# Kernel optimization log

Measured on AMD Instinct MI355X. Metric: run time of the kernel, lower is better.

The kernel has to match this reference:

```python
import jax, jax.numpy as jnp
import numpy as np

CONF_THRES = 0.1
IOU_THRES = 0.6
MAX_DET = 300
MAX_WH = 4096.0  # class offset for non-agnostic NMS
NEG_SLOPE = 0.01  # nn.LeakyReLU default


def xywh2xyxy(p):
    xy, wh = p[..., :2], p[..., 2:4]
    return jnp.concatenate([xy - wh / 2, xy + wh / 2], axis=-1)


def pairwise_iou(a, b):
    area_a = (a[:, 2] - a[:, 0]) * (a[:, 3] - a[:, 1])
    area_b = (b[:, 2] - b[:, 0]) * (b[:, 3] - b[:, 1])
    lt = jnp.maximum(a[:, None, :2], b[None, :, :2])
    rb = jnp.minimum(a[:, None, 2:], b[None, :, 2:])
    wh = jnp.clip(rb - lt, 0.0)
    inter = wh[..., 0] * wh[..., 1]
    return inter / (area_a[:, None] + area_b[None, :] - inter + 1e-7)


def nms_single(pred):  # pred: [N, 5+nc]
    boxes = xywh2xyxy(pred[:, :4])
    scores = pred[:, 5:] * pred[:, 4:5]  # obj * cls
    conf = jnp.max(scores, axis=1)
    cls = jnp.argmax(scores, axis=1)
    conf = jnp.where(conf > CONF_THRES, conf, 0.0)
    topv, topi = jax.lax.top_k(conf, MAX_DET)
    b = boxes[topi]                      # [K,4]
    c = cls[topi]
    valid = topv > CONF_THRES
    bo = b + (c.astype(b.dtype) * MAX_WH)[:, None]  # class-offset boxes
    iou = pairwise_iou(bo, bo)           # [K,K]
    idx = jnp.arange(MAX_DET)
    def body(i, keep):
        sup = keep[i] & (iou[i] > IOU_THRES) & (idx > i)
        return keep & ~sup
    keep = jax.lax.fori_loop(0, MAX_DET, body, valid)
    return b, keep


def bilinear_sample(feat, y, x):  # feat [C,H,W], y/x [K,P] -> [C,K,P]
    C, H, W = feat.shape
    y = jnp.clip(y, 0.0, H - 1.0)
    x = jnp.clip(x, 0.0, W - 1.0)
    y0 = jnp.floor(y).astype(jnp.int32)
    x0 = jnp.floor(x).astype(jnp.int32)
    y1 = jnp.minimum(y0 + 1, H - 1)
    x1 = jnp.minimum(x0 + 1, W - 1)
    ly = y - y0
    lx = x - x0
    return (feat[:, y0, x0] * ((1 - ly) * (1 - lx))
            + feat[:, y0, x1] * ((1 - ly) * lx)
            + feat[:, y1, x0] * (ly * (1 - lx))
            + feat[:, y1, x1] * (ly * lx))


def roi_align_1x1(feat, boxes, scale):  # feat [C,H,W], boxes [K,4] xyxy (input-px)
    b = boxes * scale
    w = jnp.maximum(b[:, 2] - b[:, 0], 1.0)
    h = jnp.maximum(b[:, 3] - b[:, 1], 1.0)
    off = jnp.array([0.5, 1.5], dtype=boxes.dtype)
    xs = b[:, 0:1] + off[None, :] * (w[:, None] / 2.0)  # [K,2]
    ys = b[:, 1:2] + off[None, :] * (h[:, None] / 2.0)
    yy = ys[:, jnp.array([0, 0, 1, 1])]  # [K,4] 2x2 grid
    xx = xs[:, jnp.array([0, 1, 0, 1])]
    v = bilinear_sample(feat, yy, xx)    # [C,K,4]
    return jnp.mean(v, axis=2).T         # [K,C]


def rescale_boxes(bbox, hw, hw0):  # scale_coords + normalize by orig shape
    gain = jnp.minimum(hw[0] / hw0[0], hw[1] / hw0[1])
    pad_x = (hw[1] - hw0[1] * gain) / 2.0
    pad_y = (hw[0] - hw0[0] * gain) / 2.0
    x1 = jnp.clip((bbox[:, 0] - pad_x) / gain, 0.0, hw0[1])
    y1 = jnp.clip((bbox[:, 1] - pad_y) / gain, 0.0, hw0[0])
    x2 = jnp.clip((bbox[:, 2] - pad_x) / gain, 0.0, hw0[1])
    y2 = jnp.clip((bbox[:, 3] - pad_y) / gain, 0.0, hw0[0])
    # divide by shapes[i][0] indexed [w,h,w,h]
    return jnp.stack([x1 / hw0[1], y1 / hw0[0], x2 / hw0[1], y2 / hw0[0]], axis=1)


def setup_inputs() -> dict:
    key = jax.random.key(0)
    ks = jax.random.split(key, 10)
    B, N, NC = 8, 25500, 80
    xy = jax.random.uniform(ks[0], (B, N, 2), minval=0.0, maxval=640.0)
    wh = jax.random.uniform(ks[1], (B, N, 2), minval=8.0, maxval=160.0)
    obj = jax.random.uniform(ks[2], (B, N, 1))
    cls = jax.random.uniform(ks[3], (B, N, NC))
    preds = jnp.concatenate([xy, wh, obj, cls], axis=-1)
    feat1 = jax.random.normal(ks[4], (B, 128, 80, 80), dtype=jnp.float32)
    feat2 = jax.random.normal(ks[5], (B, 256, 40, 40), dtype=jnp.float32)
    feat3 = jax.random.normal(ks[6], (B, 512, 20, 20), dtype=jnp.float32)
    feat4 = jax.random.normal(ks[7], (B, 1024, 10, 10), dtype=jnp.float32)
    orig_hw = jnp.tile(jnp.array([[720.0, 1280.0]], dtype=jnp.float32), (B, 1))
    W1 = jax.random.normal(ks[8], (1920, 256), dtype=jnp.float32) * 0.02
    b1 = jnp.zeros((256,), dtype=jnp.float32)
    W2 = jax.random.normal(ks[9], (256, 256), dtype=jnp.float32) * 0.02
    b2 = jnp.zeros((256,), dtype=jnp.float32)
    return {"preds": preds, "feat1": feat1, "feat2": feat2, "feat3": feat3,
            "feat4": feat4, "orig_hw": orig_hw, "W1": W1, "b1": b1,
            "W2": W2, "b2": b2}


def reference(preds, feat1, feat2, feat3, feat4, orig_hw, W1, b1, W2, b2):
    preds = jax.lax.stop_gradient(preds)  # out.detach() in the original
    hw = jnp.array(feat1.shape[-2:], dtype=preds.dtype) * 8.0  # network input h,w
    boxes, keep = jax.vmap(nms_single)(preds)  # [B,K,4], [B,K]
    f1 = jax.vmap(lambda f, b: roi_align_1x1(f, b, 1.0 / 8))(feat1, boxes)
    f2 = jax.vmap(lambda f, b: roi_align_1x1(f, b, 1.0 / 16))(feat2, boxes)
    f3 = jax.vmap(lambda f, b: roi_align_1x1(f, b, 1.0 / 32))(feat3, boxes)
    f4 = jax.vmap(lambda f, b: roi_align_1x1(f, b, 1.0 / 64))(feat4, boxes)
    f = jnp.concatenate([f1, f2, f3, f4], axis=-1)  # [B,K,1920]
    h = jax.nn.leaky_relu(f @ W1 + b1, NEG_SLOPE)
    h = jax.nn.leaky_relu(h @ W2 + b2, NEG_SLOPE)   # [B,K,256]
    bb = jax.vmap(lambda b, s: rescale_boxes(b, hw, s))(boxes, orig_hw)
    out = jnp.concatenate([bb, h], axis=-1)  # [B,K,260]
    return out * keep[..., None].astype(out.dtype)
```

## Files before the change

### kernel.cpp

```cpp
#include <hip/hip_runtime.h>
#include <hip/hip_bf16.h>
#include <cstdint>
#include <cstddef>

#define NBATCH 8
#define NANCH 25500
#define MAXDET 300
#define NBINS 2048
#define NMS_BLKS 8
#define SCAT_BLKS 64
#define TRANS_BASE (NMS_BLKS + SCAT_BLKS)
#define TRANS_BLKS 376

typedef __bf16 bf16x8 __attribute__((ext_vector_type(8)));
typedef float floatx4 __attribute__((ext_vector_type(4)));
typedef unsigned long long ull;

__device__ __forceinline__ int conf_bin(float v) {
  unsigned bits = __float_as_uint(v);
  int bin = (int)((bits - 0x3D800000u) >> 14);
  return bin > (NBINS - 1) ? (NBINS - 1) : bin;
}

#define CONF_TILE 64
__global__ __launch_bounds__(256) void conf_kernel(const float* __restrict__ preds,
                                                   float* __restrict__ conf,
                                                   int* __restrict__ cls,
                                                   int* __restrict__ ghist, int total) {
  __shared__ float s[CONF_TILE * 85];
  int base = blockIdx.x * CONF_TILE;
  int nA = total - base; if (nA > CONF_TILE) nA = CONF_TILE;
  int n4 = (nA * 85) >> 2;
  const float4* g4 = (const float4*)(preds + (size_t)base * 85);
  float4* s4 = (float4*)s;
  for (int i = threadIdx.x; i < n4; i += 256) s4[i] = g4[i];
  __syncthreads();
  int lane16 = threadIdx.x & 15;
  int sub = threadIdx.x >> 4;
  #pragma unroll
  for (int r = 0; r < 4; ++r) {
    int a = r * 16 + sub;
    if (a < nA) {
      const float* row = s + a * 85;
      float obj = row[4];
      float best = -1.0f; int bc = 0;
      #pragma unroll
      for (int j = 0; j < 5; ++j) {
        int c = lane16 * 5 + j;
        float v = row[5 + c] * obj;
        if (v > best) { best = v; bc = c; }
      }
      #pragma unroll
      for (int m = 1; m < 16; m <<= 1) {
        float ov = __shfl_xor(best, m, 64);
        int   oc = __shfl_xor(bc,   m, 64);
        if (ov > best || (ov == best && oc < bc)) { best = ov; bc = oc; }
      }
      if (lane16 == 0) {
        int idx = base + a;
        bool pass = best > 0.1f;
        conf[idx] = pass ? best : 0.0f;
        cls[idx] = bc;
        if (pass) {
          int b = idx / NANCH;
          atomicAdd(&ghist[b * NBINS + conf_bin(best)], 1);
        }
      }
    }
  }
}

struct TransArgs {
  const float* src[6];
  __hip_bfloat16* dst[6];
  int C[6], HW[6], tx[6], tpb[6], start[6];
};

__global__ __launch_bounds__(1024) void mid_kernel(TransArgs a,
                                                   const float* __restrict__ conf,
                                                   const float* __restrict__ preds,
                                                   const int* __restrict__ clsg,
                                                   const int* __restrict__ ghist,
                                                   int* __restrict__ gcnt,
                                                   int* __restrict__ ctr2,
                                                   ull* __restrict__ gA,
                                                   ull* __restrict__ gB,
                                                   ull* __restrict__ gC,
                                                   float* __restrict__ boxesWs, int* __restrict__ keepWs,
                                                   const float* __restrict__ orig_hw,
                                                   float* __restrict__ out,
                                                   int n_trans_tiles) {
  #pragma clang fp contract(off)
  __shared__ __align__(16) char smem[69632];
  int bid = blockIdx.x;
  int t = threadIdx.y * 32 + threadIdx.x;

  if (bid >= TRANS_BASE) {
    int wv = t >> 6, l = t & 63;
    int wid = (bid - TRANS_BASE) * 16 + wv;
    int wtot = ((int)gridDim.x - TRANS_BASE) * 16;
    float* tile = (float*)(smem + wv * 4352);
    for (int gt = wid; gt < n_trans_tiles; gt += wtot) {
      int s = 0;
      #pragma unroll
      for (int i = 1; i < 6; ++i) if (gt >= a.start[i]) s = i;
      int local = gt - a.start[s];
      int C = a.C[s], HW = a.HW[s], tx0 = a.tx[s], tpb = a.tpb[s];
      int bb = local / tpb;
      int rem = local - bb * tpb;
      int p0 = (rem % tx0) * 32;
      int c0 = (rem / tx0) * 32;
      const float* inb = a.src[s] + (size_t)bb * C * HW;
      __hip_bfloat16* outb = a.dst[s] + (size_t)bb * C * HW;
      if (p0 + 32 <= HW) {
        #pragma unroll
        for (int k = 0; k < 4; ++k) {
          int cr = k * 8 + (l >> 3);
          int pr = (l & 7) * 4;
          float4 v = *(const float4*)(inb + (size_t)(c0 + cr) * HW + p0 + pr);
          float* d = tile + cr * 33 + pr;
          d[0] = v.x; d[1] = v.y; d[2] = v.z; d[3] = v.w;
        }
        asm volatile("s_waitcnt lgkmcnt(0)" ::: "memory");
        __builtin_amdgcn_sched_barrier(0);
        #pragma unroll
        for (int k = 0; k < 16; ++k) {
          int pr = k * 2 + (l >> 5);
          int cr = l & 31;
          outb[(size_t)(p0 + pr) * C + c0 + cr] = __float2bfloat16(tile[cr * 33 + pr]);
        }
      } else {
        int nvp = HW - p0;
        #pragma unroll
        for (int k = 0; k < 4; ++k) {
          int cr = k * 8 + (l >> 3);
          int pr = (l & 7) * 4;
          const float* src = inb + (size_t)(c0 + cr) * HW + p0;
          float* d = tile + cr * 33 + pr;
          #pragma unroll
          for (int j = 0; j < 4; ++j) d[j] = (pr + j < nvp) ? src[pr + j] : 0.0f;
        }
        asm volatile("s_waitcnt lgkmcnt(0)" ::: "memory");
        __builtin_amdgcn_sched_barrier(0);
        #pragma unroll
        for (int k = 0; k < 16; ++k) {
          int pr = k * 2 + (l >> 5);
          int cr = l & 31;
          if (pr < nvp) outb[(size_t)(p0 + pr) * C + c0 + cr] = __float2bfloat16(tile[cr * 33 + pr]);
        }
      }
    }
    return;
  }

  if (bid >= NMS_BLKS) {
    int hb = bid - NMS_BLKS;
    int b = hb >> 3, seg = hb & 7;
    int* s_suf = (int*)smem;
    int* shv   = (int*)(smem + 8192);
    int r[8], suf[8], rs[8];
    int w = t >> 6, lane = t & 63;
    if (t == 0) shv[0] = NBINS;
    if (t < 256) {
      #pragma unroll
      for (int k = 0; k < 8; ++k)
        r[k] = ghist[b * NBINS + (w * 8 + k) * 64 + lane];
      int bsum = 0;
      #pragma unroll
      for (int k = 0; k < 8; ++k) {
        int s = r[k];
        #pragma unroll
        for (int d = 1; d < 64; d <<= 1) {
          int o = __shfl_down(s, d, 64);
          if (lane + d < 64) s += o;
        }
        suf[k] = s - r[k];
        rs[k] = __shfl(s, 0, 64);
        bsum += rs[k];
      }
      if (lane == 0) shv[4 + w] = bsum;
    }
    __syncthreads();
    if (t < 256) {
      int p1 = shv[5], p2 = shv[6], p3 = shv[7];
      int total = shv[4] + p1 + p2 + p3;
      int target = total < 300 ? total : 300;
      int RS = (w == 0) ? (p1 + p2 + p3) : (w == 1) ? (p2 + p3) : (w == 2) ? p3 : 0;
      int run = RS;
      #pragma unroll
      for (int k = 7; k >= 0; --k) {
        int Sx = run + suf[k] + r[k];
        int Sx1 = Sx - r[k];
        int bin = (w * 8 + k) * 64 + lane;
        s_suf[bin] = Sx1;
        if (total > 0 && Sx >= target && Sx1 < target) shv[0] = bin;
        run += rs[k];
      }
    }
    __syncthreads();
    int T = shv[0];
    const int N4 = NANCH >> 2;
    int i0 = (N4 * seg) >> 3, i1 = (N4 * (seg + 1)) >> 3;
    const float4* cf4 = (const float4*)(conf + (size_t)b * NANCH);
    for (int i = i0 + t; i < i1; i += 1024) {
      float4 v4 = cf4[i];
      int ib = i * 4;
      float vv[4] = {v4.x, v4.y, v4.z, v4.w};
      #pragma unroll
      for (int q = 0; q < 4; ++q) {
        float v = vv[q];
        if (v > 0.1f) {
          int bin = conf_bin(v);
          if (bin >= T) {
            int slot = s_suf[bin] + atomicAdd(&gcnt[b * NBINS + bin], 1);
            int idx = ib + q;
            const float* p = preds + ((size_t)b * NANCH + idx) * 85;
            float cx = p[0], cy = p[1], wq = p[2], hq = p[3];
            float hw2 = wq * 0.5f, hh2 = hq * 0.5f;
            float x1 = cx - hw2, y1 = cy - hh2, x2 = cx + hw2, y2 = cy + hh2;
            int c = clsg[(size_t)b * NANCH + idx];
            size_t g = (size_t)b * NANCH + slot;
            atomicExch(&gA[g], ((ull)__float_as_uint(v) << 32) | (unsigned)(idx | (c << 20)));
            atomicExch(&gB[g], ((ull)__float_as_uint(x1) << 32) | __float_as_uint(y1));
            atomicExch(&gC[g], ((ull)__float_as_uint(x2) << 32) | __float_as_uint(y2));
          }
        }
      }
    }
    __syncthreads();
    if (t == 0) { __threadfence(); atomicAdd(&ctr2[b], 1); }
    return;
  }

  int b = bid;
  int*    s_h  = (int*)smem;
  float4* bo4  = (float4*)(smem + 8192);
  float (*bxx)[4] = (float(*)[4])(smem + 12992);
  ull   (*mask)[5] = (ull(*)[5])(smem + 17792);
  ull* keepw = (ull*)(smem + 29792);
  ull* nzrow = (ull*)(smem + 29832);
  int* shv   = (int*)(smem + 29872);

  if (t < 300) {
    bo4[t] = make_float4(0.0f, 0.0f, 0.0f, 0.0f);
    bxx[t][0] = 0.0f; bxx[t][1] = 0.0f; bxx[t][2] = 0.0f; bxx[t][3] = 0.0f;
  }
  if (t < 5) nzrow[t] = 0ULL;
  if (t == 0) { shv[0] = NBINS; shv[2] = 0; }
  {
    int r[8], suf[8], rs[8];
    int w = t >> 6, lane = t & 63;
    if (t < 256) {
      #pragma unroll
      for (int k = 0; k < 8; ++k)
        r[k] = ghist[b * NBINS + (w * 8 + k) * 64 + lane];
      int bsum = 0;
      #pragma unroll
      for (int k = 0; k < 8; ++k) {
        int s = r[k];
        #pragma unroll
        for (int d = 1; d < 64; d <<= 1) {
          int o = __shfl_down(s, d, 64);
          if (lane + d < 64) s += o;
        }
        suf[k] = s - r[k];
        rs[k] = __shfl(s, 0, 64);
        bsum += rs[k];
      }
      if (lane == 0) shv[4 + w] = bsum;
    }
    __syncthreads();
    if (t < 256) {
      int p1 = shv[5], p2 = shv[6], p3 = shv[7];
      int total = shv[4] + p1 + p2 + p3;
      int target = total < 300 ? total : 300;
      int RS = (w == 0) ? (p1 + p2 + p3) : (w == 1) ? (p2 + p3) : (w == 2) ? p3 : 0;
      int run = RS;
      #pragma unroll
      for (int k = 7; k >= 0; --k) {
        int Sx = run + suf[k] + r[k];
        int Sx1 = Sx - r[k];
        int bin = (w * 8 + k) * 64 + lane;
        s_h[bin] = Sx;
        if (total > 0 && Sx >= target && Sx1 < target) { shv[0] = bin; shv[2] = Sx; }
        run += rs[k];
      }
      if (t == 0) shv[1] = total;
    }
  }
  __syncthreads();
  int total = shv[1];
  int Kslots = shv[2];
  int nvalid = total < 300 ? total : 300;

  if (t >= nvalid && t < 300) {
    size_t bi = ((size_t)(b * 300 + t)) * 4;
    boxesWs[bi + 0] = 0.0f; boxesWs[bi + 1] = 0.0f;
    boxesWs[bi + 2] = 0.0f; boxesWs[bi + 3] = 0.0f;
  }
  if (t < 5) {
    int n = nvalid - t * 64;
    keepw[t] = (n <= 0) ? 0ULL : (n >= 64 ? ~0ULL : ((1ULL << n) - 1ULL));
  }
  if (t == 0) {
    while (atomicAdd(&ctr2[b], 0) < 8) __builtin_amdgcn_s_sleep(8);
    __threadfence();
  }
  __syncthreads();

  for (int sIdx = t; sIdx < Kslots; sIdx += 1024) {
    ull aA = atomicAdd(&gA[(size_t)b * NANCH + sIdx], 0ULL);
    float v = __uint_as_float((unsigned)(aA >> 32));
    unsigned code = (unsigned)aA;
    int id = (int)(code & 0xFFFFFu);
    int bin = conf_bin(v);
    int lo = (bin + 1 < NBINS) ? s_h[bin + 1] : 0;
    int hi = s_h[bin];
    int rank = lo;
    #pragma unroll 4
    for (int j = lo; j < hi; ++j) {
      ull aj = atomicAdd(&gA[(size_t)b * NANCH + j], 0ULL);
      float vj = __uint_as_float((unsigned)(aj >> 32));
      int ij = (int)((unsigned)aj & 0xFFFFFu);
      int gt = vj > v;
      int eq = (vj == v) & (ij < id);
      rank += gt | eq;
    }
    if (rank < 300) {
      ull pb = atomicAdd(&gB[(size_t)b * NANCH + sIdx], 0ULL);
      ull pc = atomicAdd(&gC[(size_t)b * NANCH + sIdx], 0ULL);
      float x1 = __uint_as_float((unsigned)(pb >> 32));
      float y1 = __uint_as_float((unsigned)pb);
      float x2 = __uint_as_float((unsigned)(pc >> 32));
      float y2 = __uint_as_float((unsigned)pc);
      bxx[rank][0] = x1; bxx[rank][1] = y1; bxx[rank][2] = x2; bxx[rank][3] = y2;
      size_t bi = ((size_t)(b * 300 + rank)) * 4;
      boxesWs[bi + 0] = x1; boxesWs[bi + 1] = y1;
      boxesWs[bi + 2] = x2; boxesWs[bi + 3] = y2;
      int c = (int)((code >> 20) & 0x7Fu);
      float off = (float)c * 4096.0f;
      float4 ob; ob.x = x1 + off; ob.y = y1 + off; ob.z = x2 + off; ob.w = y2 + off;
      bo4[rank] = ob;
    }
  }
  __syncthreads();

  {
    int wv2 = t >> 6, ln = t & 63;
    if (wv2 < 10) {
      int w2 = wv2 >> 1, half = wv2 & 1;
      int j = w2 * 64 + ln;
      int jc = j < 300 ? j : 0;
      float4 jb = bo4[jc];
      float ja = (jb.z - jb.x) * (jb.w - jb.y);
      bool jv = j < 300;
      int iend = w2 * 64 + 64; if (iend > 300) iend = 300;
      int i0 = half * 150, i1 = i0 + 150; if (i1 > iend) i1 = iend;
      #pragma unroll 4
      for (int i = i0; i < i1; ++i) {
        float4 ib = bo4[i];
        float ai = (ib.z - ib.x) * (ib.w - ib.y);
        float ltx = fmaxf(ib.x, jb.x);
        float lty = fmaxf(ib.y, jb.y);
        float rbx = fminf(ib.z, jb.z);
        float rby = fminf(ib.w, jb.w);
        float wx = fmaxf(rbx - ltx, 0.0f);
        float wy = fmaxf(rby - lty, 0.0f);
        float inter = wx * wy;
        float iou = inter / (ai + ja - inter + 1e-7f);
        ull bal = __ballot(jv && (j > i) && (iou > 0.6f));
        if (ln == 0) {
          mask[i][w2] = bal;
          if (bal) atomicOr(&nzrow[i >> 6], 1ULL << (i & 63));
        }
      }
    }
  }
  __syncthreads();
  if (t == 0) {
    ull kw[5], nz[5];
    #pragma unroll
    for (int w2 = 0; w2 < 5; ++w2) { kw[w2] = keepw[w2]; nz[w2] = nzrow[w2]; }
    #pragma unroll
    for (int w2 = 0; w2 < 5; ++w2) {
      ull p = kw[w2] & nz[w2];
      while (p) {
        int l2 = __builtin_ctzll(p);
        p &= p - 1;
        int i = w2 * 64 + l2;
        for (int w3 = w2; w3 < 5; ++w3) {
          ull m = mask[i][w3];
          kw[w3] &= ~m;
          if (w3 == w2) p &= ~m;
        }
      }
    }
    #pragma unroll
    for (int w2 = 0; w2 < 5; ++w2) keepw[w2] = kw[w2];
  }
  __syncthreads();
  if (t < 300) {
    int kp = (int)((keepw[t >> 6] >> (t & 63)) & 1ULL);
    keepWs[b * 300 + t] = kp;
    float oh = orig_hw[b * 2 + 0], ow = orig_hw[b * 2 + 1];
    float gain = fminf(640.0f / oh, 640.0f / ow);
    float padx = (640.0f - ow * gain) * 0.5f;
    float pady = (640.0f - oh * gain) * 0.5f;
    float x1 = fminf(fmaxf((bxx[t][0] - padx) / gain, 0.0f), ow) / ow;
    float y1 = fminf(fmaxf((bxx[t][1] - pady) / gain, 0.0f), oh) / oh;
    float x2 = fminf(fmaxf((bxx[t][2] - padx) / gain, 0.0f), ow) / ow;
    float y2 = fminf(fmaxf((bxx[t][3] - pady) / gain, 0.0f), oh) / oh;
    size_t o = ((size_t)(b * 300 + t)) * 260;
    out[o + 0] = kp ? x1 : 0.0f;
    out[o + 1] = kp ? y1 : 0.0f;
    out[o + 2] = kp ? x2 : 0.0f;
    out[o + 3] = kp ? y2 : 0.0f;
  }
}

__global__ __launch_bounds__(256) void roi_kernel(const float* __restrict__ boxes,
                                                  const __hip_bfloat16* __restrict__ fT1, const __hip_bfloat16* __restrict__ fT2,
                                                  const __hip_bfloat16* __restrict__ fT3, const __hip_bfloat16* __restrict__ fT4,
                                                  __hip_bfloat16* __restrict__ f) {
  int b = blockIdx.x & 7;
  int r = blockIdx.x >> 3;
  __shared__ int t_off[4][16];
  __shared__ float t_w[4][16];
  int t = threadIdx.x;
  const int Hs[4] = {80, 40, 20, 10};
  const int Cs[4] = {128, 256, 512, 1024};
  const float ss[4] = {0.125f, 0.0625f, 0.03125f, 0.015625f};
  size_t bbase = ((size_t)(b * 300 + r)) * 4;
  float bx0 = boxes[bbase + 0];
  float by0 = boxes[bbase + 1];
  float bx1 = boxes[bbase + 2];
  float by1 = boxes[bbase + 3];
  if (t < 64) {
    int lv = t >> 4, k = t & 15, pp = k >> 2, nb = k & 3;
    float s = ss[lv];
    int H = Hs[lv], W = Hs[lv], C = Cs[lv];
    float b0 = bx0 * s, b1 = by0 * s, b2 = bx1 * s, b3 = by1 * s;
    float w = fmaxf(b2 - b0, 1.0f), h = fmaxf(b3 - b1, 1.0f);
    const float offv[2] = {0.5f, 1.5f};
    float px = b0 + offv[pp & 1] * (w * 0.5f);
    float py = b1 + offv[pp >> 1] * (h * 0.5f);
    float y = fminf(fmaxf(py, 0.0f), (float)(H - 1));
    float x = fminf(fmaxf(px, 0.0f), (float)(W - 1));
    int y0 = (int)floorf(y), x0 = (int)floorf(x);
    int y1 = min(y0 + 1, H - 1), x1 = min(x0 + 1, W - 1);
    float ly = y - (float)y0, lx = x - (float)x0;
    int yy = (nb & 2) ? y1 : y0;
    int xx = (nb & 1) ? x1 : x0;
    float wy = (nb & 2) ? ly : (1.0f - ly);
    float wx = (nb & 1) ? lx : (1.0f - lx);
    t_off[lv][k] = (yy * W + xx) * C;
    t_w[lv][k] = wy * wx;
  }
  __syncthreads();
  const __hip_bfloat16* bases[4] = {
    fT1 + (size_t)b * 6400 * 128,
    fT2 + (size_t)b * 1600 * 256,
    fT3 + (size_t)b * 400 * 512,
    fT4 + (size_t)b * 100 * 1024
  };
  __hip_bfloat16* frow = f + (size_t)(b * 300 + r) * 1920;
  int cbase = 0;
  #pragma unroll
  for (int lv = 0; lv < 4; ++lv) {
    int C = Cs[lv];
    const __hip_bfloat16* base = bases[lv];
    for (int c = t; c < C; c += 256) {
      float acc = 0.0f;
      #pragma unroll
      for (int k = 0; k < 16; ++k)
        acc += t_w[lv][k] * __bfloat162float(base[t_off[lv][k] + c]);
      frow[cbase + c] = __float2bfloat16(acc * 0.25f);
    }
    cbase += C;
  }
}

#define GLDS16(gp, lp) __builtin_amdgcn_global_load_lds( \
    (const __attribute__((address_space(1))) unsigned int*)(gp), \
    (__attribute__((address_space(3))) unsigned int*)(lp), 16, 0, 0)

__global__ __launch_bounds__(256) void gemm_tile_kernel(const __hip_bfloat16* __restrict__ A,
                                                        const __hip_bfloat16* __restrict__ BT,
                                                        const float* __restrict__ bias,
                                                        __hip_bfloat16* __restrict__ Cb,
                                                        float* __restrict__ Cf,
                                                        const int* __restrict__ keep,
                                                        int M, int N, int K, int ldc, int coff) {
  __shared__ __hip_bfloat16 sA[2][64 * 64];
  __shared__ __hip_bfloat16 sB[2][64 * 64];
  int tid = threadIdx.x;
  int bm = blockIdx.x * 64, bn = blockIdx.y * 64;
  int wave = tid >> 6, lane = tid & 63;
  int wr = wave >> 1, wc = wave & 1;
  int idx16 = lane & 15, kb = lane >> 4;
  floatx4 acc[2][2] = {};
  int nt = K >> 6;

  auto stage = [&](int buf, int t) {
    int k0 = t << 6;
    #pragma unroll
    for (int i = 0; i < 2; ++i) {
      int c = tid + i * 256;
      int row = c >> 3, cc = c & 7;
      int scc = cc ^ (row & 7);
      GLDS16(A + (size_t)(bm + row) * K + k0 + scc * 8,
             (char*)&sA[buf][0] + c * 16);
    }
    #pragma unroll
    for (int i = 0; i < 2; ++i) {
      int c = tid + i * 256;
      int row = c >> 3, cc = c & 7;
      int scc = cc ^ (row & 7);
      GLDS16(BT + (size_t)(bn + row) * K + k0 + scc * 8,
             (char*)&sB[buf][0] + c * 16);
    }
  };

  stage(0, 0);
  asm volatile("s_waitcnt vmcnt(0)" ::: "memory");
  __syncthreads();
  int cur = 0;
  for (int t = 0; t < nt; ++t) {
    if (t + 1 < nt) stage(cur ^ 1, t + 1);
    const char* Ab = (const char*)&sA[cur][0];
    const char* Bb = (const char*)&sB[cur][0];
    #pragma unroll
    for (int s = 0; s < 2; ++s) {
      bf16x8 af[2], bg[2];
      #pragma unroll
      for (int m = 0; m < 2; ++m) {
        int row = wr * 32 + m * 16 + idx16;
        int chunk = s * 4 + kb;
        af[m] = *(const bf16x8*)(Ab + row * 128 + ((chunk ^ (row & 7)) * 16));
      }
      #pragma unroll
      for (int n = 0; n < 2; ++n) {
        int row = wc * 32 + n * 16 + idx16;
        int chunk = s * 4 + kb;
        bg[n] = *(const bf16x8*)(Bb + row * 128 + ((chunk ^ (row & 7)) * 16));
      }
      #pragma unroll
      for (int m = 0; m < 2; ++m)
        #pragma unroll
        for (int n = 0; n < 2; ++n)
          acc[m][n] = __builtin_amdgcn_mfma_f32_16x16x32_bf16(af[m], bg[n], acc[m][n], 0, 0, 0);
    }
    asm volatile("s_waitcnt vmcnt(0)" ::: "memory");
    __syncthreads();
    cur ^= 1;
  }
  int col = lane & 15, rb4 = (lane >> 4) * 4;
  #pragma unroll
  for (int m = 0; m < 2; ++m) {
    #pragma unroll
    for (int n = 0; n < 2; ++n) {
      #pragma unroll
      for (int r = 0; r < 4; ++r) {
        int orow = bm + wr * 32 + m * 16 + rb4 + r;
        int ocol = bn + wc * 32 + n * 16 + col;
        if (orow >= M) continue;
        float v = acc[m][n][r] + bias[ocol];
        v = (v >= 0.0f) ? v : 0.01f * v;
        if (Cb) Cb[(size_t)orow * N + ocol] = __float2bfloat16(v);
        if (Cf) {
          float km = keep ? (keep[orow] ? 1.0f : 0.0f) : 1.0f;
          Cf[(size_t)orow * ldc + coff + ocol] = v * km;
        }
      }
    }
  }
}

extern "C" void kernel_launch(void* const* d_in, const int* in_sizes, int n_in,
                              void* d_out, int out_size, void* d_ws, size_t ws_size,
                              hipStream_t stream) {
  (void)in_sizes; (void)n_in; (void)out_size; (void)ws_size;
  const float* preds  = (const float*)d_in[0];
  const float* feat1  = (const float*)d_in[1];
  const float* feat2  = (const float*)d_in[2];
  const float* feat3  = (const float*)d_in[3];
  const float* feat4  = (const float*)d_in[4];
  const float* orighw = (const float*)d_in[5];
  const float* W1     = (const float*)d_in[6];
  const float* b1     = (const float*)d_in[7];
  const float* W2     = (const float*)d_in[8];
  const float* b2     = (const float*)d_in[9];
  float* out = (float*)d_out;

  char* ws = (char*)d_ws;
  size_t off = 0;
  auto alloc = [&](size_t bytes) -> void* {
    void* p = ws + off;
    off = (off + bytes + 255) & ~(size_t)255;
    return p;
  };
  const int BN = NBATCH * NANCH;
  float*  conf   = (float*)alloc((size_t)BN * 4);
  int*    cls    = (int*)  alloc((size_t)BN * 4);
  ull*    gA     = (ull*)  alloc((size_t)BN * 8);
  ull*    gB     = (ull*)  alloc((size_t)BN * 8);
  ull*    gC     = (ull*)  alloc((size_t)BN * 8);
  int*    ghist  = (int*)  alloc((size_t)NBATCH * NBINS * 4);
  int*    gcnt   = (int*)  alloc((size_t)NBATCH * NBINS * 4);
  int*    ctr2   = (int*)  alloc(256);
  float*  boxes  = (float*)alloc((size_t)NBATCH * 300 * 4 * 4);
  int*    keep   = (int*)  alloc((size_t)NBATCH * 300 * 4);
  __hip_bfloat16* fT1  = (__hip_bfloat16*)alloc((size_t)NBATCH * 6400 * 128 * 2);
  __hip_bfloat16* fT2  = (__hip_bfloat16*)alloc((size_t)NBATCH * 1600 * 256 * 2);
  __hip_bfloat16* fT3  = (__hip_bfloat16*)alloc((size_t)NBATCH * 400 * 512 * 2);
  __hip_bfloat16* fT4  = (__hip_bfloat16*)alloc((size_t)NBATCH * 100 * 1024 * 2);
  __hip_bfloat16* fmat = (__hip_bfloat16*)alloc((size_t)2400 * 1920 * 2);
  __hip_bfloat16* h1b  = (__hip_bfloat16*)alloc((size_t)2400 * 256 * 2);
  __hip_bfloat16* W1T  = (__hip_bfloat16*)alloc((size_t)256 * 1920 * 2);
  __hip_bfloat16* W2T  = (__hip_bfloat16*)alloc((size_t)256 * 256 * 2);

  hipMemsetAsync(ghist, 0, (size_t)NBATCH * NBINS * 4 * 2 + 256, stream);

  conf_kernel<<<(BN + CONF_TILE - 1) / CONF_TILE, 256, 0, stream>>>(preds, conf, cls, ghist, BN);

  TransArgs ta;
  ta.src[0] = feat1; ta.dst[0] = fT1; ta.C[0] = 128;  ta.HW[0] = 6400; ta.tx[0] = 200;
  ta.src[1] = feat2; ta.dst[1] = fT2; ta.C[1] = 256;  ta.HW[1] = 1600; ta.tx[1] = 50;
  ta.src[2] = feat3; ta.dst[2] = fT3; ta.C[2] = 512;  ta.HW[2] = 400;  ta.tx[2] = 13;
  ta.src[3] = feat4; ta.dst[3] = fT4; ta.C[3] = 1024; ta.HW[3] = 100;  ta.tx[3] = 4;
  ta.src[4] = W1;    ta.dst[4] = W1T; ta.C[4] = 1920; ta.HW[4] = 256;  ta.tx[4] = 8;
  ta.src[5] = W2;    ta.dst[5] = W2T; ta.C[5] = 256;  ta.HW[5] = 256;  ta.tx[5] = 8;
  int n_tiles = 0;
  for (int s = 0; s < 6; ++s) {
    int ty = (ta.C[s] + 31) / 32;
    int nbatch = (s < 4) ? NBATCH : 1;
    ta.tpb[s] = ta.tx[s] * ty;
    ta.start[s] = n_tiles;
    n_tiles += ta.tpb[s] * nbatch;
  }
  mid_kernel<<<TRANS_BASE + TRANS_BLKS, dim3(32, 32), 0, stream>>>(ta, conf, preds, cls,
                                                                   ghist, gcnt, ctr2,
                                                                   gA, gB, gC,
                                                                   boxes, keep, orighw, out,
                                                                   n_tiles);

  roi_kernel<<<2400, 256, 0, stream>>>(boxes, fT1, fT2, fT3, fT4, fmat);
  gemm_tile_kernel<<<dim3(38, 4), 256, 0, stream>>>(fmat, W1T, b1, h1b, nullptr, nullptr,
                                                    2400, 256, 1920, 0, 0);
  gemm_tile_kernel<<<dim3(38, 4), 256, 0, stream>>>(h1b, W2T, b2, nullptr, out, keep,
                                                    2400, 256, 256, 260, 4);
}
```

Measured before the change: 135.6 us.

## Split fused mid kernel into scatter/transpose and separate NMS kernel

The single persistent mid kernel, which ran NMS, scatter and feature transposes in one launch with a spin-wait counter between blocks, is split into a transpose+scatter kernel and a separate NMS kernel ordered by the stream. The scatter now writes plain SoA arrays (value, index, float4 box) instead of packed 64-bit atomicExch, and NMS reads them with normal loads instead of atomic reads. The transpose moves to one 32x32 tile per 256-thread block with a simpler grid. This removes atomic traffic and the spin-wait, at the cost of an extra launch and losing the overlap between NMS setup and the transposes.

Measured after the change: 145.2 us. 7.0% more time.

```diff
diff --git a/kernel.cpp b/kernel.cpp
--- a/kernel.cpp
+++ b/kernel.cpp
@@ -7,10 +7,7 @@
 #define NANCH 25500
 #define MAXDET 300
 #define NBINS 2048
-#define NMS_BLKS 8
 #define SCAT_BLKS 64
-#define TRANS_BASE (NMS_BLKS + SCAT_BLKS)
-#define TRANS_BLKS 376
 
 typedef __bf16 bf16x8 __attribute__((ext_vector_type(8)));
 typedef float floatx4 __attribute__((ext_vector_type(4)));
@@ -76,92 +73,28 @@
   int C[6], HW[6], tx[6], tpb[6], start[6];
 };
 
-__global__ __launch_bounds__(1024) void mid_kernel(TransArgs a,
-                                                   const float* __restrict__ conf,
-                                                   const float* __restrict__ preds,
-                                                   const int* __restrict__ clsg,
-                                                   const int* __restrict__ ghist,
-                                                   int* __restrict__ gcnt,
-                                                   int* __restrict__ ctr2,
-                                                   ull* __restrict__ gA,
-                                                   ull* __restrict__ gB,
-                                                   ull* __restrict__ gC,
-                                                   float* __restrict__ boxesWs, int* __restrict__ keepWs,
-                                                   const float* __restrict__ orig_hw,
-                                                   float* __restrict__ out,
-                                                   int n_trans_tiles) {
+__global__ __launch_bounds__(256) void trans_scatter_kernel(TransArgs a,
+                                                            const float* __restrict__ conf,
+                                                            const float* __restrict__ preds,
+                                                            const int* __restrict__ clsg,
+                                                            const int* __restrict__ ghist,
+                                                            int* __restrict__ gcnt,
+                                                            float* __restrict__ gV,
+                                                            int* __restrict__ gI,
+                                                            float4* __restrict__ gBox) {
   #pragma clang fp contract(off)
-  __shared__ __align__(16) char smem[69632];
+  __shared__ __align__(16) char smem[8448];
   int bid = blockIdx.x;
   int t = threadIdx.y * 32 + threadIdx.x;
 
-  if (bid >= TRANS_BASE) {
-    int wv = t >> 6, l = t & 63;
-    int wid = (bid - TRANS_BASE) * 16 + wv;
-    int wtot = ((int)gridDim.x - TRANS_BASE) * 16;
-    float* tile = (float*)(smem + wv * 4352);
-    for (int gt = wid; gt < n_trans_tiles; gt += wtot) {
-      int s = 0;
-      #pragma unroll
-      for (int i = 1; i < 6; ++i) if (gt >= a.start[i]) s = i;
-      int local = gt - a.start[s];
-      int C = a.C[s], HW = a.HW[s], tx0 = a.tx[s], tpb = a.tpb[s];
-      int bb = local / tpb;
-      int rem = local - bb * tpb;
-      int p0 = (rem % tx0) * 32;
-      int c0 = (rem / tx0) * 32;
-      const float* inb = a.src[s] + (size_t)bb * C * HW;
-      __hip_bfloat16* outb = a.dst[s] + (size_t)bb * C * HW;
-      if (p0 + 32 <= HW) {
-        #pragma unroll
-        for (int k = 0; k < 4; ++k) {
-          int cr = k * 8 + (l >> 3);
-          int pr = (l & 7) * 4;
-          float4 v = *(const float4*)(inb + (size_t)(c0 + cr) * HW + p0 + pr);
-          float* d = tile + cr * 33 + pr;
-          d[0] = v.x; d[1] = v.y; d[2] = v.z; d[3] = v.w;
-        }
-        asm volatile("s_waitcnt lgkmcnt(0)" ::: "memory");
-        __builtin_amdgcn_sched_barrier(0);
-        #pragma unroll
-        for (int k = 0; k < 16; ++k) {
-          int pr = k * 2 + (l >> 5);
-          int cr = l & 31;
-          outb[(size_t)(p0 + pr) * C + c0 + cr] = __float2bfloat16(tile[cr * 33 + pr]);
-        }
-      } else {
-        int nvp = HW - p0;
-        #pragma unroll
-        for (int k = 0; k < 4; ++k) {
-          int cr = k * 8 + (l >> 3);
-          int pr = (l & 7) * 4;
-          const float* src = inb + (size_t)(c0 + cr) * HW + p0;
-          float* d = tile + cr * 33 + pr;
-          #pragma unroll
-          for (int j = 0; j < 4; ++j) d[j] = (pr + j < nvp) ? src[pr + j] : 0.0f;
-        }
-        asm volatile("s_waitcnt lgkmcnt(0)" ::: "memory");
-        __builtin_amdgcn_sched_barrier(0);
-        #pragma unroll
-        for (int k = 0; k < 16; ++k) {
-          int pr = k * 2 + (l >> 5);
-          int cr = l & 31;
-          if (pr < nvp) outb[(size_t)(p0 + pr) * C + c0 + cr] = __float2bfloat16(tile[cr * 33 + pr]);
-        }
-      }
-    }
-    return;
-  }
-
-  if (bid >= NMS_BLKS) {
-    int hb = bid - NMS_BLKS;
-    int b = hb >> 3, seg = hb & 7;
+  if (bid < SCAT_BLKS) {
+    int b = bid >> 3, seg = bid & 7;
     int* s_suf = (int*)smem;
     int* shv   = (int*)(smem + 8192);
     int r[8], suf[8], rs[8];
     int w = t >> 6, lane = t & 63;
     if (t == 0) shv[0] = NBINS;
-    if (t < 256) {
+    {
       #pragma unroll
       for (int k = 0; k < 8; ++k)
         r[k] = ghist[b * NBINS + (w * 8 + k) * 64 + lane];
@@ -181,7 +114,7 @@
       if (lane == 0) shv[4 + w] = bsum;
     }
     __syncthreads();
-    if (t < 256) {
+    {
       int p1 = shv[5], p2 = shv[6], p3 = shv[7];
       int total = shv[4] + p1 + p2 + p3;
       int target = total < 300 ? total : 300;
@@ -202,7 +135,7 @@
     const int N4 = NANCH >> 2;
     int i0 = (N4 * seg) >> 3, i1 = (N4 * (seg + 1)) >> 3;
     const float4* cf4 = (const float4*)(conf + (size_t)b * NANCH);
-    for (int i = i0 + t; i < i1; i += 1024) {
+    for (int i = i0 + t; i < i1; i += 256) {
       float4 v4 = cf4[i];
       int ib = i * 4;
       float vv[4] = {v4.x, v4.y, v4.z, v4.w};
@@ -220,19 +153,54 @@
             float x1 = cx - hw2, y1 = cy - hh2, x2 = cx + hw2, y2 = cy + hh2;
             int c = clsg[(size_t)b * NANCH + idx];
             size_t g = (size_t)b * NANCH + slot;
-            atomicExch(&gA[g], ((ull)__float_as_uint(v) << 32) | (unsigned)(idx | (c << 20)));
-            atomicExch(&gB[g], ((ull)__float_as_uint(x1) << 32) | __float_as_uint(y1));
-            atomicExch(&gC[g], ((ull)__float_as_uint(x2) << 32) | __float_as_uint(y2));
+            gV[g] = v;
+            gI[g] = idx | (c << 20);
+            gBox[g] = make_float4(x1, y1, x2, y2);
           }
         }
       }
     }
+    return;
+  }
+
+  {
+    float (*tile)[33] = (float(*)[33])smem;
+    int bid2 = bid - SCAT_BLKS;
+    int s = 0;
+    #pragma unroll
+    for (int i = 1; i < 6; ++i) if (bid2 >= a.start[i]) s = i;
+    int local = bid2 - a.start[s];
+    int C = a.C[s], HW = a.HW[s], tx0 = a.tx[s], tpb = a.tpb[s];
+    int b = local / tpb;
+    int rem = local - b * tpb;
+    int p0 = (rem % tx0) * 32;
+    int c0 = (rem / tx0) * 32;
+    const float* inb = a.src[s] + (size_t)b * C * HW;
+    __hip_bfloat16* outb = a.dst[s] + (size_t)b * C * HW;
+    int tx = threadIdx.x, ty = threadIdx.y;
+    #pragma unroll
+    for (int k = 0; k < 32; k += 8) {
+      int c = c0 + ty + k, p = p0 + tx;
+      if (c < C && p < HW) tile[ty + k][tx] = inb[(size_t)c * HW + p];
+    }
     __syncthreads();
-    if (t == 0) { __threadfence(); atomicAdd(&ctr2[b], 1); }
-    return;
-  }
-
-  int b = bid;
+    #pragma unroll
+    for (int k = 0; k < 32; k += 8) {
+      int p = p0 + ty + k, c = c0 + tx;
+      if (p < HW && c < C) outb[(size_t)p * C + c] = __float2bfloat16(tile[tx][ty + k]);
+    }
+  }
+}
+
+__global__ __launch_bounds__(1024) void nms_kernel(const float* __restrict__ gV,
+                                                   const int* __restrict__ gI,
+                                                   const float4* __restrict__ gBox,
+                                                   const int* __restrict__ ghist,
+                                                   float* __restrict__ boxesWs, int* __restrict__ keepWs,
+                                                   const float* __restrict__ orig_hw,
+                                                   float* __restrict__ out) {
+  #pragma clang fp contract(off)
+  __shared__ __align__(16) char smem[30208];
   int*    s_h  = (int*)smem;
   float4* bo4  = (float4*)(smem + 8192);
   float (*bxx)[4] = (float(*)[4])(smem + 12992);
@@ -240,6 +208,8 @@
   ull* keepw = (ull*)(smem + 29792);
   ull* nzrow = (ull*)(smem + 29832);
   int* shv   = (int*)(smem + 29872);
+  int b = blockIdx.x;
+  int t = threadIdx.x;
 
   if (t < 300) {
     bo4[t] = make_float4(0.0f, 0.0f, 0.0f, 0.0f);
@@ -302,45 +272,36 @@
     int n = nvalid - t * 64;
     keepw[t] = (n <= 0) ? 0ULL : (n >= 64 ? ~0ULL : ((1ULL << n) - 1ULL));
   }
-  if (t == 0) {
-    while (atomicAdd(&ctr2[b], 0) < 8) __builtin_amdgcn_s_sleep(8);
-    __threadfence();
-  }
-  __syncthreads();
-
-  for (int sIdx = t; sIdx < Kslots; sIdx += 1024) {
-    ull aA = atomicAdd(&gA[(size_t)b * NANCH + sIdx], 0ULL);
-    float v = __uint_as_float((unsigned)(aA >> 32));
-    unsigned code = (unsigned)aA;
-    int id = (int)(code & 0xFFFFFu);
-    int bin = conf_bin(v);
-    int lo = (bin + 1 < NBINS) ? s_h[bin + 1] : 0;
-    int hi = s_h[bin];
-    int rank = lo;
-    #pragma unroll 4
-    for (int j = lo; j < hi; ++j) {
-      ull aj = atomicAdd(&gA[(size_t)b * NANCH + j], 0ULL);
-      float vj = __uint_as_float((unsigned)(aj >> 32));
-      int ij = (int)((unsigned)aj & 0xFFFFFu);
-      int gt = vj > v;
-      int eq = (vj == v) & (ij < id);
-      rank += gt | eq;
-    }
-    if (rank < 300) {
-      ull pb = atomicAdd(&gB[(size_t)b * NANCH + sIdx], 0ULL);
-      ull pc = atomicAdd(&gC[(size_t)b * NANCH + sIdx], 0ULL);
-      float x1 = __uint_as_float((unsigned)(pb >> 32));
-      float y1 = __uint_as_float((unsigned)pb);
-      float x2 = __uint_as_float((unsigned)(pc >> 32));
-      float y2 = __uint_as_float((unsigned)pc);
-      bxx[rank][0] = x1; bxx[rank][1] = y1; bxx[rank][2] = x2; bxx[rank][3] = y2;
-      size_t bi = ((size_t)(b * 300 + rank)) * 4;
-      boxesWs[bi + 0] = x1; boxesWs[bi + 1] = y1;
-      boxesWs[bi + 2] = x2; boxesWs[bi + 3] = y2;
-      int c = (int)((code >> 20) & 0x7Fu);
-      float off = (float)c * 4096.0f;
-      float4 ob; ob.x = x1 + off; ob.y = y1 + off; ob.z = x2 + off; ob.w = y2 + off;
-      bo4[rank] = ob;
+
+  {
+    const float* vb = gV + (size_t)b * NANCH;
+    const int*   ib2 = gI + (size_t)b * NANCH;
+    for (int sIdx = t; sIdx < Kslots; sIdx += 1024) {
+      float v = vb[sIdx];
+      unsigned code = (unsigned)ib2[sIdx];
+      int id = (int)(code & 0xFFFFFu);
+      int bin = conf_bin(v);
+      int lo = (bin + 1 < NBINS) ? s_h[bin + 1] : 0;
+      int hi = s_h[bin];
+      int rank = lo;
+      for (int j = lo; j < hi; ++j) {
+        float vj = vb[j];
+        int ij = ib2[j] & 0xFFFFF;
+        int gt = vj > v;
+        int eq = (vj == v) & (ij < id);
+        rank += gt | eq;
+      }
+      if (rank < 300) {
+        float4 bx = gBox[(size_t)b * NANCH + sIdx];
+        bxx[rank][0] = bx.x; bxx[rank][1] = bx.y; bxx[rank][2] = bx.z; bxx[rank][3] = bx.w;
+        size_t bi = ((size_t)(b * 300 + rank)) * 4;
+        boxesWs[bi + 0] = bx.x; boxesWs[bi + 1] = bx.y;
+        boxesWs[bi + 2] = bx.z; boxesWs[bi + 3] = bx.w;
+        int c = (int)(code >> 20);
+        float off = (float)c * 4096.0f;
+        float4 ob; ob.x = bx.x + off; ob.y = bx.y + off; ob.z = bx.z + off; ob.w = bx.w + off;
+        bo4[rank] = ob;
+      }
     }
   }
   __syncthreads();
@@ -602,12 +563,11 @@
   const int BN = NBATCH * NANCH;
   float*  conf   = (float*)alloc((size_t)BN * 4);
   int*    cls    = (int*)  alloc((size_t)BN * 4);
-  ull*    gA     = (ull*)  alloc((size_t)BN * 8);
-  ull*    gB     = (ull*)  alloc((size_t)BN * 8);
-  ull*    gC     = (ull*)  alloc((size_t)BN * 8);
+  float*  gV     = (float*)alloc((size_t)BN * 4);
+  int*    gI     = (int*)  alloc((size_t)BN * 4);
+  float4* gBox   = (float4*)alloc((size_t)BN * 16);
   int*    ghist  = (int*)  alloc((size_t)NBATCH * NBINS * 4);
   int*    gcnt   = (int*)  alloc((size_t)NBATCH * NBINS * 4);
-  int*    ctr2   = (int*)  alloc(256);
   float*  boxes  = (float*)alloc((size_t)NBATCH * 300 * 4 * 4);
   int*    keep   = (int*)  alloc((size_t)NBATCH * 300 * 4);
   __hip_bfloat16* fT1  = (__hip_bfloat16*)alloc((size_t)NBATCH * 6400 * 128 * 2);
@@ -619,7 +579,7 @@
   __hip_bfloat16* W1T  = (__hip_bfloat16*)alloc((size_t)256 * 1920 * 2);
   __hip_bfloat16* W2T  = (__hip_bfloat16*)alloc((size_t)256 * 256 * 2);
 
-  hipMemsetAsync(ghist, 0, (size_t)NBATCH * NBINS * 4 * 2 + 256, stream);
+  hipMemsetAsync(ghist, 0, (size_t)NBATCH * NBINS * 4 * 2, stream);
 
   conf_kernel<<<(BN + CONF_TILE - 1) / CONF_TILE, 256, 0, stream>>>(preds, conf, cls, ghist, BN);
 
@@ -638,11 +598,11 @@
     ta.start[s] = n_tiles;
     n_tiles += ta.tpb[s] * nbatch;
   }
-  mid_kernel<<<TRANS_BASE + TRANS_BLKS, dim3(32, 32), 0, stream>>>(ta, conf, preds, cls,
-                                                                   ghist, gcnt, ctr2,
-                                                                   gA, gB, gC,
-                                                                   boxes, keep, orighw, out,
-                                                                   n_tiles);
+  trans_scatter_kernel<<<SCAT_BLKS + n_tiles, dim3(32, 8), 0, stream>>>(ta, conf, preds, cls,
+                                                                        ghist, gcnt,
+                                                                        gV, gI, gBox);
+
+  nms_kernel<<<NBATCH, 1024, 0, stream>>>(gV, gI, gBox, ghist, boxes, keep, orighw, out);
 
   roi_kernel<<<2400, 256, 0, stream>>>(boxes, fT1, fT2, fT3, fT4, fmat);
   gemm_tile_kernel<<<dim3(38, 4), 256, 0, stream>>>(fmat, W1T, b1, h1b, nullptr, nullptr,
```
